# Kernel tuning notes

Measured on AMD Instinct MI355X. Metric: run time of the kernel, lower is better.

The kernel has to match this reference:

```python
import jax, jax.numpy as jnp
import numpy as np


def setup_inputs() -> dict:
    key = jax.random.key(0)
    k1, k2, k3, k4, k5, k6 = jax.random.split(key, 6)
    B, HID, SP, H, W = 256, 1024, 2048, 14, 14
    hidden = jax.random.normal(k1, (B, HID), dtype=jnp.float32)
    spatial_features = jax.random.normal(k2, (B, SP, H, W), dtype=jnp.float32)
    # attention MLP params: Linear(hid+sp -> hid), Tanh, Linear(hid -> 1)
    s1 = 1.0 / np.sqrt(HID + SP)
    W1 = jax.random.uniform(k3, (HID + SP, HID), dtype=jnp.float32, minval=-s1, maxval=s1)
    b1 = jax.random.uniform(k4, (HID,), dtype=jnp.float32, minval=-s1, maxval=s1)
    s2 = 1.0 / np.sqrt(HID)
    W2 = jax.random.uniform(k5, (HID, 1), dtype=jnp.float32, minval=-s2, maxval=s2)
    b2 = jax.random.uniform(k6, (1,), dtype=jnp.float32, minval=-s2, maxval=s2)
    return {"hidden": hidden, "spatial_features": spatial_features,
            "W1": W1, "b1": b1, "W2": W2, "b2": b2}


def reference(hidden, spatial_features, W1, b1, W2, b2):
    B, C, H, W = spatial_features.shape
    # [B, H*W, C]
    sp = spatial_features.reshape(B, C, H * W).transpose(0, 2, 1)
    hid = hidden[:, None, :]  # [B, 1, HID]
    # Split the concat-matmul: [hid|sp] @ W1 == hid @ W1_h + sp @ W1_s
    HID = hidden.shape[1]
    W1h, W1s = W1[:HID], W1[HID:]
    pre = jnp.einsum('bh,hd->bd', hidden, W1h)[:, None, :] \
        + jnp.einsum('bnc,cd->bnd', sp, W1s) + b1  # [B, HW, HID]
    scores = jnp.einsum('bnd,d->bn', jnp.tanh(pre), W2[:, 0]) + b2[0]  # [B, HW]
    attn = jax.nn.softmax(scores, axis=1)
    context = jnp.einsum('bn,bnc->bc', attn, sp)  # [B, C]
    return context, attn
```

## Files before the change

### kernel.cpp

```cpp
#include <hip/hip_runtime.h>
#include <hip/hip_bf16.h>
#include <hip/hip_fp16.h>
#include <math.h>

#define B_   256
#define HID_ 1024
#define SP_  2048
#define N_   196
#define NJ_  (B_ * N_)
#define SPB_ (SP_ * N_)

typedef float    f32x4 __attribute__((ext_vector_type(4)));
typedef _Float16 f16x8 __attribute__((ext_vector_type(8)));

#define GLOBAL_AS(p) ((const __attribute__((address_space(1))) void*)(p))
#define LDS_AS(p)    ((__attribute__((address_space(3))) void*)(p))

__device__ __forceinline__ float fast_tanh(float x) {
    const float e = exp2f(x * 2.8853900817779268f);
    return 1.f - 2.f / (e + 1.f);
}

__global__ __launch_bounds__(256) void k1_h1(
    const float* __restrict__ hidden, const float* __restrict__ W1,
    const float* __restrict__ b1, float* __restrict__ h1)
{
    __shared__ float hs[4][HID_];
    const int t = threadIdx.x;
    const int d = blockIdx.x * 256 + t;
    const int b0 = blockIdx.y * 4;

    for (int i = t; i < 4 * HID_; i += 256)
        hs[i >> 10][i & 1023] = hidden[(size_t)(b0 + (i >> 10)) * HID_ + (i & 1023)];
    __syncthreads();

    float acc[4] = {};
    for (int h = 0; h < HID_; ++h) {
        const float w = W1[(size_t)h * HID_ + d];
#pragma unroll
        for (int i = 0; i < 4; ++i) acc[i] += hs[i][h] * w;
    }
    const float bias = b1[d];
#pragma unroll
    for (int i = 0; i < 4; ++i)
        h1[(size_t)(b0 + i) * HID_ + d] = acc[i] + bias;
}

__global__ __launch_bounds__(256) void k0a_packA(
    const float* __restrict__ W1, __half* __restrict__ Ah)
{
    const size_t idx = (size_t)blockIdx.x * 256 + threadIdx.x;
    const int c8 = idx & 7;
    const int dd = (idx >> 3) & 127;
    const int cg = (idx >> 10) & 3;
    const int ks = (idx >> 12) & 63;
    const int dt = idx >> 18;
    const int d = dt * 128 + dd;
    const int c = ks * 32 + cg * 8 + c8;
    Ah[idx] = __float2half(W1[(size_t)(HID_ + c) * HID_ + d]);
}

__global__ __launch_bounds__(256) void k0b_packB(
    const float* __restrict__ spatial, __half* __restrict__ Bh)
{
    const int jt2 = blockIdx.x;
    const int ks  = blockIdx.y;
    const int jj  = threadIdx.x;

    const int j = jt2 * 256 + jj;
    const int b = j / N_;
    const int n = j - b * N_;
    const float* spj = spatial + (size_t)b * SPB_ + n;
    __half* outb = Bh + (((size_t)jt2 * 64 + ks) * 4) * 2048 + jj * 8;

#pragma unroll
    for (int cg = 0; cg < 4; ++cg) {
        const float* src = spj + (size_t)(ks * 32 + cg * 8) * N_;
        f16x8 v;
#pragma unroll
        for (int c8 = 0; c8 < 8; ++c8)
            v[c8] = (_Float16)src[(size_t)c8 * N_];
        *(f16x8*)(outb + (size_t)cg * 2048) = v;
    }
}

__global__ __launch_bounds__(256, 2) void k2_pipe(
    const __half* __restrict__ Ah, const __half* __restrict__ Bh,
    const float* __restrict__ W2, const float* __restrict__ h1,
    float* __restrict__ ps)
{
    extern __shared__ __align__(16) short ldsb[];

    const int tid = threadIdx.x;
    const int l  = tid & 63;
    const int w  = tid >> 6;
    const int wm = w >> 1;
    const int wn = w & 1;
    const int cg = l >> 4;
    const int rr = l & 15;

    const int orig = blockIdx.x;
    const int wgid = (orig & 7) * 196 + (orig >> 3);
    const int jt2 = wgid >> 3;
    const int dt  = wgid & 7;

    const __half* apack = Ah + ((size_t)dt * 64) * 4096;
    const __half* bpack = Bh + ((size_t)jt2 * 64) * 8192;

    f32x4 acc[4][8] = {};

#define STAGE_A(KT, SLOT) do {                                                  \
        const __half* as_ = apack + (size_t)(KT) * 4096;                        \
        short* ad_ = ldsb + (SLOT) * 12288 + w * 1024;                          \
        __builtin_amdgcn_global_load_lds(GLOBAL_AS(as_ + w * 1024 + l * 8),     \
                                         LDS_AS(ad_), 16, 0, 0);                \
        __builtin_amdgcn_global_load_lds(GLOBAL_AS(as_ + w * 1024 + 512 + l * 8),\
                                         LDS_AS(ad_ + 512), 16, 0, 0);          \
    } while (0)

#define STAGE_B(KT, SLOT) do {                                                  \
        const __half* bs_ = bpack + (size_t)(KT) * 8192;                        \
        short* bd_ = ldsb + (SLOT) * 12288 + 4096 + w * 2048;                   \
        _Pragma("unroll")                                                       \
        for (int i_ = 0; i_ < 4; ++i_)                                          \
            __builtin_amdgcn_global_load_lds(                                   \
                GLOBAL_AS(bs_ + w * 2048 + i_ * 512 + l * 8),                   \
                LDS_AS(bd_ + i_ * 512), 16, 0, 0);                              \
    } while (0)

#define STEP(KT, CSLOT, SSLOT, DO_STAGE, VMC) do {                              \
        const short* ab_ = ldsb + (CSLOT) * 12288;                              \
        const short* bb_ = ab_ + 4096;                                          \
        f16x8 af[2], bf[8], af2[2];                                             \
        _Pragma("unroll")                                                       \
        for (int ni = 0; ni < 8; ++ni)                                          \
            bf[ni] = *(const f16x8*)&bb_[(cg * 256 + wn * 128 + ni * 16 + rr) * 8];\
        _Pragma("unroll")                                                       \
        for (int mi = 0; mi < 2; ++mi)                                          \
            af[mi] = *(const f16x8*)&ab_[(cg * 128 + wm * 64 + mi * 16 + rr) * 8];\
        if (DO_STAGE) STAGE_A((KT) + 2, SSLOT);                                 \
        __builtin_amdgcn_s_barrier();                                           \
        asm volatile("s_waitcnt lgkmcnt(0)" ::: "memory");                      \
        __builtin_amdgcn_sched_barrier(0);                                      \
        __builtin_amdgcn_s_setprio(1);                                          \
        _Pragma("unroll")                                                       \
        for (int mi = 0; mi < 2; ++mi)                                          \
            _Pragma("unroll")                                                   \
            for (int ni = 0; ni < 8; ++ni)                                      \
                acc[mi][ni] = __builtin_amdgcn_mfma_f32_16x16x32_f16(           \
                    af[mi], bf[ni], acc[mi][ni], 0, 0, 0);                      \
        __builtin_amdgcn_s_setprio(0);                                          \
        _Pragma("unroll")                                                       \
        for (int mi = 0; mi < 2; ++mi)                                          \
            af2[mi] = *(const f16x8*)&ab_[(cg * 128 + wm * 64 + (mi + 2) * 16 + rr) * 8];\
        if (DO_STAGE) STAGE_B((KT) + 2, SSLOT);                                 \
        asm volatile("s_waitcnt vmcnt(" #VMC ")" ::: "memory");                 \
        __builtin_amdgcn_s_barrier();                                           \
        asm volatile("s_waitcnt lgkmcnt(0)" ::: "memory");                      \
        __builtin_amdgcn_sched_barrier(0);                                      \
        __builtin_amdgcn_s_setprio(1);                                          \
        _Pragma("unroll")                                                       \
        for (int mi = 0; mi < 2; ++mi)                                          \
            _Pragma("unroll")                                                   \
            for (int ni = 0; ni < 8; ++ni)                                      \
                acc[mi + 2][ni] = __builtin_amdgcn_mfma_f32_16x16x32_f16(       \
                    af2[mi], bf[ni], acc[mi + 2][ni], 0, 0, 0);                 \
        __builtin_amdgcn_s_setprio(0);                                          \
    } while (0)

    STAGE_A(0, 0); STAGE_B(0, 0);
    STAGE_A(1, 1); STAGE_B(1, 1);
    asm volatile("s_waitcnt vmcnt(6)" ::: "memory");
    __builtin_amdgcn_s_barrier();

#pragma unroll 1
    for (int kt = 0; kt < 60; kt += 3) {
        STEP(kt + 0, 0, 2, true, 6);
        STEP(kt + 1, 1, 0, true, 6);
        STEP(kt + 2, 2, 1, true, 6);
    }
    STEP(60, 0, 2, true, 6);
    STEP(61, 1, 0, true, 6);
    STEP(62, 2, 0, false, 0);
    STEP(63, 0, 0, false, 0);

#undef STAGE_A
#undef STAGE_B
#undef STEP

    const int dbase = dt * 128 + wm * 64;
    float w2v[4][4];
#pragma unroll
    for (int mi = 0; mi < 4; ++mi)
#pragma unroll
        for (int q = 0; q < 4; ++q)
            w2v[mi][q] = W2[dbase + mi * 16 + cg * 4 + q];

    float partial[8];
#pragma unroll
    for (int ni = 0; ni < 8; ++ni) {
        const int j = jt2 * 256 + wn * 128 + ni * 16 + rr;
        const int bj = j / N_;
        const float* h1p = h1 + (size_t)bj * HID_ + dbase;
        float s = 0.f;
#pragma unroll
        for (int mi = 0; mi < 4; ++mi)
#pragma unroll
            for (int q = 0; q < 4; ++q)
                s += fast_tanh(acc[mi][ni][q] + h1p[mi * 16 + cg * 4 + q]) * w2v[mi][q];
        partial[ni] = s;
    }

    float* red = (float*)ldsb;
    __syncthreads();
    red[tid] = 0.f;
    __syncthreads();
#pragma unroll
    for (int ni = 0; ni < 8; ++ni)
        atomicAdd(&red[wn * 128 + ni * 16 + rr], partial[ni]);
    __syncthreads();
    ps[(size_t)dt * NJ_ + (size_t)jt2 * 256 + tid] = red[tid];
}

__global__ __launch_bounds__(256) void k2_fb(
    const float* __restrict__ spatial, const float* __restrict__ W1,
    const float* __restrict__ W2, const float* __restrict__ h1,
    float* __restrict__ ps)
{
    __shared__ float As[32][64];
    __shared__ float Bs[32][64];
    const int t = threadIdx.x;
    const int d0 = blockIdx.x * 64;
    const int j0 = blockIdx.y * 64;
    const int ld = t & 63, lk = t >> 6;
    const float* Aptr = W1 + (size_t)(HID_ + lk) * HID_ + (d0 + ld);
    const int j = j0 + ld;
    const int bb = j / N_, nn = j - bb * N_;
    const float* Bptr = spatial + (size_t)bb * SPB_ + (size_t)lk * N_ + nn;
    const int tr = t >> 4, tc = t & 15;
    float acc[4][4] = {};
    for (int c0 = 0; c0 < SP_; c0 += 32) {
#pragma unroll
        for (int i = 0; i < 8; ++i) {
            As[lk + 4 * i][ld] = Aptr[(size_t)(c0 + 4 * i) * HID_];
            Bs[lk + 4 * i][ld] = Bptr[(size_t)(c0 + 4 * i) * N_];
        }
        __syncthreads();
#pragma unroll
        for (int k = 0; k < 32; ++k) {
            float av[4], bv[4];
            *(float4*)av = *(const float4*)&As[k][tr * 4];
            *(float4*)bv = *(const float4*)&Bs[k][tc * 4];
#pragma unroll
            for (int di = 0; di < 4; ++di)
#pragma unroll
                for (int ji = 0; ji < 4; ++ji)
                    acc[di][ji] += av[di] * bv[ji];
        }
        __syncthreads();
    }
    float w2v[4];
#pragma unroll
    for (int di = 0; di < 4; ++di) w2v[di] = W2[d0 + tr * 4 + di];
    float partial[4] = {};
#pragma unroll
    for (int ji = 0; ji < 4; ++ji) {
        const int jg = j0 + tc * 4 + ji;
        const int bj = jg / N_;
        const float* h1row = h1 + (size_t)bj * HID_ + d0 + tr * 4;
#pragma unroll
        for (int di = 0; di < 4; ++di)
            partial[ji] += tanhf(acc[di][ji] + h1row[di]) * w2v[di];
    }
    __shared__ float red[64];
    if (t < 64) red[t] = 0.f;
    __syncthreads();
#pragma unroll
    for (int ji = 0; ji < 4; ++ji)
        atomicAdd(&red[tc * 4 + ji], partial[ji]);
    __syncthreads();
    if (t < 64)
        ps[(size_t)blockIdx.x * NJ_ + j0 + t] = red[t];
}

__global__ __launch_bounds__(256) void k3_softmax(
    const float* __restrict__ ps, float* __restrict__ attn, int nslices)
{
    const int b = blockIdx.x;
    const int t = threadIdx.x;
    __shared__ float sdata[256];

    float s = -1e30f;
    if (t < N_) {
        s = 0.f;
        for (int dt = 0; dt < nslices; ++dt)
            s += ps[(size_t)dt * NJ_ + b * N_ + t];
    }
    sdata[t] = s;
    __syncthreads();
    for (int off = 128; off > 0; off >>= 1) {
        if (t < off) sdata[t] = fmaxf(sdata[t], sdata[t + off]);
        __syncthreads();
    }
    const float m = sdata[0];
    __syncthreads();
    const float e = (t < N_) ? expf(s - m) : 0.f;
    sdata[t] = e;
    __syncthreads();
    for (int off = 128; off > 0; off >>= 1) {
        if (t < off) sdata[t] += sdata[t + off];
        __syncthreads();
    }
    const float inv = 1.f / sdata[0];
    if (t < N_) attn[(size_t)b * N_ + t] = e * inv;
}

__global__ __launch_bounds__(256) void k4_context(
    const float* __restrict__ spatial, const float* __restrict__ attn,
    float* __restrict__ ctx)
{
    const int wid = (blockIdx.x * 256 + threadIdx.x) >> 6;
    const int lane = threadIdx.x & 63;
    const int b = wid >> 11;
    const int c = wid & 2047;
    const float* sp = spatial + (size_t)b * SPB_ + (size_t)c * N_;
    const float* at = attn + (size_t)b * N_;

    float sum = 0.f;
    if (lane < 49) {
        const float4 s4 = ((const float4*)sp)[lane];
        const float4 a4 = ((const float4*)at)[lane];
        sum = s4.x * a4.x + s4.y * a4.y + s4.z * a4.z + s4.w * a4.w;
    }
#pragma unroll
    for (int off = 32; off > 0; off >>= 1)
        sum += __shfl_down(sum, off, 64);
    if (lane == 0)
        ctx[(size_t)b * 2048 + c] = sum;
}

extern "C" void kernel_launch(void* const* d_in, const int* in_sizes, int n_in,
                              void* d_out, int out_size, void* d_ws, size_t ws_size,
                              hipStream_t stream)
{
    const float* hidden  = (const float*)d_in[0];
    const float* spatial = (const float*)d_in[1];
    const float* W1      = (const float*)d_in[2];
    const float* b1      = (const float*)d_in[3];
    const float* W2      = (const float*)d_in[4];

    float* out_ctx  = (float*)d_out;
    float* out_attn = (float*)d_out + (size_t)B_ * 2048;

    char* ws = (char*)d_ws;
    float* h1 = (float*)ws;
    float* psb = (float*)(ws + (1u << 20));

    const size_t offAh = 8u << 20;
    const size_t offBh = 16u << 20;
    const size_t szB   = (size_t)196 * 64 * 8192 * 2;
    const size_t needed = offBh + szB;

    k1_h1<<<dim3(4, 64), 256, 0, stream>>>(hidden, W1, b1, h1);

    if (ws_size >= needed) {
        __half* Ah = (__half*)(ws + offAh);
        __half* Bh = (__half*)(ws + offBh);
        k0a_packA<<<dim3(8192), 256, 0, stream>>>(W1, Ah);
        k0b_packB<<<dim3(196, 64), 256, 0, stream>>>(spatial, Bh);
        (void)hipFuncSetAttribute((const void*)k2_pipe,
                                  hipFuncAttributeMaxDynamicSharedMemorySize,
                                  73728);
        k2_pipe<<<dim3(1568), 256, 73728, stream>>>(Ah, Bh, W2, h1, psb);
        k3_softmax<<<dim3(B_), 256, 0, stream>>>(psb, out_attn, 8);
    } else {
        k2_fb<<<dim3(16, 784), 256, 0, stream>>>(spatial, W1, W2, h1, psb);
        k3_softmax<<<dim3(B_), 256, 0, stream>>>(psb, out_attn, 16);
    }
    k4_context<<<dim3((B_ * 2048) / 4), 256, 0, stream>>>(spatial, out_attn, out_ctx);
}
```

Measured before the change: 517.1 us.

## Load A operand directly into registers, keep only B in LDS

The GEMM pipeline stops staging the W1 (A) tiles through LDS and instead loads each wave's A fragments straight from global memory into double-buffered registers one k-step ahead. The B tile pipeline stays triple-buffered in LDS, now in a smaller static allocation, and the dynamic shared memory attribute call is removed. The aim is to cut LDS traffic and footprint, and drop one lgkmcnt wait per step. In exchange it raises register pressure and exposes the A global-load latency, now covered only by register double buffering.

After: 562.6 us. 1.09x slower.

```diff
diff --git a/kernel.cpp b/kernel.cpp
--- a/kernel.cpp
+++ b/kernel.cpp
@@ -89,7 +89,7 @@
     const float* __restrict__ W2, const float* __restrict__ h1,
     float* __restrict__ ps)
 {
-    extern __shared__ __align__(16) short ldsb[];
+    __shared__ __align__(16) short ldsb[3 * 8192];
 
     const int tid = threadIdx.x;
     const int l  = tid & 63;
@@ -108,19 +108,19 @@
     const __half* bpack = Bh + ((size_t)jt2 * 64) * 8192;
 
     f32x4 acc[4][8] = {};
-
-#define STAGE_A(KT, SLOT) do {                                                  \
-        const __half* as_ = apack + (size_t)(KT) * 4096;                        \
-        short* ad_ = ldsb + (SLOT) * 12288 + w * 1024;                          \
-        __builtin_amdgcn_global_load_lds(GLOBAL_AS(as_ + w * 1024 + l * 8),     \
-                                         LDS_AS(ad_), 16, 0, 0);                \
-        __builtin_amdgcn_global_load_lds(GLOBAL_AS(as_ + w * 1024 + 512 + l * 8),\
-                                         LDS_AS(ad_ + 512), 16, 0, 0);          \
+    f16x8 afr0[4], afr1[4];
+
+#define LOAD_A(KT, DST) do {                                                    \
+        const __half* aa_ = apack + (size_t)(KT) * 4096;                        \
+        _Pragma("unroll")                                                       \
+        for (int mi = 0; mi < 4; ++mi)                                          \
+            DST[mi] = *(const f16x8*)(aa_ +                                     \
+                (size_t)((cg * 128 + wm * 64 + mi * 16 + rr) * 8));             \
     } while (0)
 
 #define STAGE_B(KT, SLOT) do {                                                  \
         const __half* bs_ = bpack + (size_t)(KT) * 8192;                        \
-        short* bd_ = ldsb + (SLOT) * 12288 + 4096 + w * 2048;                   \
+        short* bd_ = ldsb + (SLOT) * 8192 + w * 2048;                           \
         _Pragma("unroll")                                                       \
         for (int i_ = 0; i_ < 4; ++i_)                                          \
             __builtin_amdgcn_global_load_lds(                                   \
@@ -128,17 +128,14 @@
                 LDS_AS(bd_ + i_ * 512), 16, 0, 0);                              \
     } while (0)
 
-#define STEP(KT, CSLOT, SSLOT, DO_STAGE, VMC) do {                              \
-        const short* ab_ = ldsb + (CSLOT) * 12288;                              \
-        const short* bb_ = ab_ + 4096;                                          \
-        f16x8 af[2], bf[8], af2[2];                                             \
+#define STEP(CSLOT, SSLOT, ACUR, ANXT, KTA, KTB, DO_LOADA, DO_STAGE, VMC) do {  \
+        const short* bb_ = ldsb + (CSLOT) * 8192;                               \
+        f16x8 bf[8];                                                            \
         _Pragma("unroll")                                                       \
         for (int ni = 0; ni < 8; ++ni)                                          \
             bf[ni] = *(const f16x8*)&bb_[(cg * 256 + wn * 128 + ni * 16 + rr) * 8];\
-        _Pragma("unroll")                                                       \
-        for (int mi = 0; mi < 2; ++mi)                                          \
-            af[mi] = *(const f16x8*)&ab_[(cg * 128 + wm * 64 + mi * 16 + rr) * 8];\
-        if (DO_STAGE) STAGE_A((KT) + 2, SSLOT);                                 \
+        if (DO_LOADA) LOAD_A(KTA, ANXT);                                        \
+        if (DO_STAGE) STAGE_B(KTB, SSLOT);                                      \
         __builtin_amdgcn_s_barrier();                                           \
         asm volatile("s_waitcnt lgkmcnt(0)" ::: "memory");                      \
         __builtin_amdgcn_sched_barrier(0);                                      \
@@ -148,15 +145,10 @@
             _Pragma("unroll")                                                   \
             for (int ni = 0; ni < 8; ++ni)                                      \
                 acc[mi][ni] = __builtin_amdgcn_mfma_f32_16x16x32_f16(           \
-                    af[mi], bf[ni], acc[mi][ni], 0, 0, 0);                      \
+                    ACUR[mi], bf[ni], acc[mi][ni], 0, 0, 0);                    \
         __builtin_amdgcn_s_setprio(0);                                          \
-        _Pragma("unroll")                                                       \
-        for (int mi = 0; mi < 2; ++mi)                                          \
-            af2[mi] = *(const f16x8*)&ab_[(cg * 128 + wm * 64 + (mi + 2) * 16 + rr) * 8];\
-        if (DO_STAGE) STAGE_B((KT) + 2, SSLOT);                                 \
         asm volatile("s_waitcnt vmcnt(" #VMC ")" ::: "memory");                 \
         __builtin_amdgcn_s_barrier();                                           \
-        asm volatile("s_waitcnt lgkmcnt(0)" ::: "memory");                      \
         __builtin_amdgcn_sched_barrier(0);                                      \
         __builtin_amdgcn_s_setprio(1);                                          \
         _Pragma("unroll")                                                       \
@@ -164,27 +156,31 @@
             _Pragma("unroll")                                                   \
             for (int ni = 0; ni < 8; ++ni)                                      \
                 acc[mi + 2][ni] = __builtin_amdgcn_mfma_f32_16x16x32_f16(       \
-                    af2[mi], bf[ni], acc[mi + 2][ni], 0, 0, 0);                 \
+                    ACUR[mi + 2], bf[ni], acc[mi + 2][ni], 0, 0, 0);            \
         __builtin_amdgcn_s_setprio(0);                                          \
     } while (0)
 
-    STAGE_A(0, 0); STAGE_B(0, 0);
-    STAGE_A(1, 1); STAGE_B(1, 1);
-    asm volatile("s_waitcnt vmcnt(6)" ::: "memory");
+    STAGE_B(0, 0);
+    LOAD_A(0, afr0);
+    STAGE_B(1, 1);
+    asm volatile("s_waitcnt vmcnt(4)" ::: "memory");
     __builtin_amdgcn_s_barrier();
 
 #pragma unroll 1
-    for (int kt = 0; kt < 60; kt += 3) {
-        STEP(kt + 0, 0, 2, true, 6);
-        STEP(kt + 1, 1, 0, true, 6);
-        STEP(kt + 2, 2, 1, true, 6);
-    }
-    STEP(60, 0, 2, true, 6);
-    STEP(61, 1, 0, true, 6);
-    STEP(62, 2, 0, false, 0);
-    STEP(63, 0, 0, false, 0);
-
-#undef STAGE_A
+    for (int kt = 0; kt < 60; kt += 6) {
+        STEP(0, 2, afr0, afr1, kt + 1, kt + 2, true, true, 4);
+        STEP(1, 0, afr1, afr0, kt + 2, kt + 3, true, true, 4);
+        STEP(2, 1, afr0, afr1, kt + 3, kt + 4, true, true, 4);
+        STEP(0, 2, afr1, afr0, kt + 4, kt + 5, true, true, 4);
+        STEP(1, 0, afr0, afr1, kt + 5, kt + 6, true, true, 4);
+        STEP(2, 1, afr1, afr0, kt + 6, kt + 7, true, true, 4);
+    }
+    STEP(0, 2, afr0, afr1, 61, 62, true, true, 4);
+    STEP(1, 0, afr1, afr0, 62, 63, true, true, 4);
+    STEP(2, 0, afr0, afr1, 63, 63, true, false, 0);
+    STEP(0, 0, afr1, afr0, 63, 63, false, false, 0);
+
+#undef LOAD_A
 #undef STAGE_B
 #undef STEP
 
@@ -368,10 +364,7 @@
         __half* Bh = (__half*)(ws + offBh);
         k0a_packA<<<dim3(8192), 256, 0, stream>>>(W1, Ah);
         k0b_packB<<<dim3(196, 64), 256, 0, stream>>>(spatial, Bh);
-        (void)hipFuncSetAttribute((const void*)k2_pipe,
-                                  hipFuncAttributeMaxDynamicSharedMemorySize,
-                                  73728);
-        k2_pipe<<<dim3(1568), 256, 73728, stream>>>(Ah, Bh, W2, h1, psb);
+        k2_pipe<<<dim3(1568), 256, 0, stream>>>(Ah, Bh, W2, h1, psb);
         k3_softmax<<<dim3(B_), 256, 0, stream>>>(psb, out_attn, 8);
     } else {
         k2_fb<<<dim3(16, 784), 256, 0, stream>>>(spatial, W1, W2, h1, psb);
```
